# Kernel tuning notes

Measured on AMD Instinct MI355X. Metric: run time of the kernel, lower is better.

Reference implementation:

```python
import jax, jax.numpy as jnp
import numpy as np

D_MODEL = 2048
N_Q = 32
N_KV = 8  # num_heads // 4
HEAD_DIM = D_MODEL // N_Q  # 64
CTX = 2048


def precompute_rope_freqs(head_dim, max_seq_len):
    theta = 1.0 / (10000.0 ** (jnp.arange(0, head_dim, 2, dtype=jnp.float32) / head_dim))
    positions = jnp.arange(max_seq_len, dtype=jnp.float32)
    return jnp.outer(positions, theta)  # [T, head_dim//2]


def apply_rope(x, freqs):
    # x: [B, T, H, D]; freqs: [T, D//2]
    T = x.shape[1]
    f = freqs[:T][None, :, None, :]  # [1, T, 1, D//2]
    cos, sin = jnp.cos(f), jnp.sin(f)
    D = x.shape[-1]
    x1, x2 = x[..., : D // 2], x[..., D // 2 :]
    return jnp.concatenate([x1 * cos - x2 * sin, x1 * sin + x2 * cos], axis=-1)


def setup_inputs() -> dict:
    key = jax.random.key(0)
    ks = jax.random.split(key, 10)
    s = 0.02
    B, T = 1, CTX
    inp = {
        "x": jax.random.normal(ks[0], (B, T, D_MODEL), dtype=jnp.float32),
        "Wq": jax.random.normal(ks[1], (D_MODEL, N_Q * HEAD_DIM), dtype=jnp.float32) * s,
        "bq": jnp.zeros((N_Q * HEAD_DIM,), dtype=jnp.float32),
        "Wk": jax.random.normal(ks[2], (D_MODEL, N_KV * HEAD_DIM), dtype=jnp.float32) * s,
        "bk": jnp.zeros((N_KV * HEAD_DIM,), dtype=jnp.float32),
        "Wv": jax.random.normal(ks[3], (D_MODEL, N_KV * HEAD_DIM), dtype=jnp.float32) * s,
        "bv": jnp.zeros((N_KV * HEAD_DIM,), dtype=jnp.float32),
        "Wo": jax.random.normal(ks[4], (D_MODEL, D_MODEL), dtype=jnp.float32) * s,
        "bo": jnp.zeros((D_MODEL,), dtype=jnp.float32),
        "freqs": precompute_rope_freqs(HEAD_DIM, CTX),
    }
    return inp


def reference(x, Wq, bq, Wk, bk, Wv, bv, Wo, bo, freqs):
    B, T, C = x.shape
    q = (x @ Wq + bq).reshape(B, T, N_Q, HEAD_DIM)
    k = (x @ Wk + bk).reshape(B, T, N_KV, HEAD_DIM)
    v = (x @ Wv + bv).reshape(B, T, N_KV, HEAD_DIM)
    q = apply_rope(q, freqs)
    k = apply_rope(k, freqs)
    repeat = N_Q // N_KV
    # repeat_interleave along head dim: q head h uses kv head h // repeat
    k = jnp.repeat(k, repeat, axis=2)
    v = jnp.repeat(v, repeat, axis=2)
    # [B, H, T, D]
    q = q.transpose(0, 2, 1, 3)
    k = k.transpose(0, 2, 1, 3)
    v = v.transpose(0, 2, 1, 3)
    scale = 1.0 / jnp.sqrt(jnp.asarray(HEAD_DIM, dtype=x.dtype))
    scores = jnp.einsum("bhtd,bhsd->bhts", q, k) * scale  # [B, H, T, T]
    causal = jnp.tril(jnp.ones((T, T), dtype=bool))
    scores = jnp.where(causal[None, None], scores, jnp.finfo(scores.dtype).min)
    attn = jax.nn.softmax(scores, axis=-1)
    out = jnp.einsum("bhts,bhsd->bhtd", attn, v)  # [B, H, T, D]
    out = out.transpose(0, 2, 1, 3).reshape(B, T, C)
    return out @ Wo + bo
```

## Files before the change

### kernel.cpp

```cpp
#include <hip/hip_runtime.h>
#include <hip/hip_bf16.h>
#include <math.h>

#define T_CTX 2048
#define DM    2048
#define NQ    32
#define NKV   8
#define HD    64
#define QKV_LD 3072

typedef __attribute__((ext_vector_type(8))) short short8;
typedef __attribute__((ext_vector_type(4))) float floatx4;

__device__ __forceinline__ void gload_lds16(const void* g, void* l) {
  __builtin_amdgcn_global_load_lds(
      (const __attribute__((address_space(1))) void*)g,
      (__attribute__((address_space(3))) void*)l, 16, 0, 0);
}

__device__ __forceinline__ void tcast_body(const float* __restrict__ src,
                                           __hip_bfloat16* __restrict__ dst,
                                           int Ncols, int Krows, int bx, int by,
                                           int tid, float (*tile)[66]) {
  const int n0 = bx * 64, k0 = by * 64;
  const int c = tid & 63, r0 = tid >> 6;
#pragma unroll
  for (int s = 0; s < 16; ++s) {
    int r = r0 + 4 * s;
    tile[r][c] = src[(size_t)(k0 + r) * Ncols + n0 + c];
  }
  __syncthreads();
#pragma unroll
  for (int s = 0; s < 16; ++s) {
    int r = r0 + 4 * s;
    dst[(size_t)(n0 + r) * Krows + k0 + c] = __float2bfloat16(tile[c][r]);
  }
}

__global__ __launch_bounds__(256) void prep_kernel(
    const float* __restrict__ x, const float* __restrict__ Wq,
    const float* __restrict__ Wk, const float* __restrict__ Wv,
    const float* __restrict__ Wo, const float* __restrict__ bq,
    const float* __restrict__ bk, const float* __restrict__ bv,
    __hip_bfloat16* __restrict__ xb, __hip_bfloat16* __restrict__ wt,
    __hip_bfloat16* __restrict__ wot, float* __restrict__ bcat) {
  __shared__ float tile[64][66];
  const int bid = blockIdx.x;
  const int tid = threadIdx.x;
  if (bid < 2048) {
    const int i = bid * 256 + tid;
    const float4 a = ((const float4*)x)[2 * i];
    const float4 b = ((const float4*)x)[2 * i + 1];
    union { ushort u[8]; short8 v; } o;
    __hip_bfloat16 h;
    h = __float2bfloat16(a.x); o.u[0] = *(ushort*)&h;
    h = __float2bfloat16(a.y); o.u[1] = *(ushort*)&h;
    h = __float2bfloat16(a.z); o.u[2] = *(ushort*)&h;
    h = __float2bfloat16(a.w); o.u[3] = *(ushort*)&h;
    h = __float2bfloat16(b.x); o.u[4] = *(ushort*)&h;
    h = __float2bfloat16(b.y); o.u[5] = *(ushort*)&h;
    h = __float2bfloat16(b.z); o.u[6] = *(ushort*)&h;
    h = __float2bfloat16(b.w); o.u[7] = *(ushort*)&h;
    ((short8*)xb)[i] = o.v;
  } else if (bid < 3072) {
    const int lid = bid - 2048;
    tcast_body(Wq, wt, 2048, 2048, lid & 31, lid >> 5, tid, tile);
  } else if (bid < 3328) {
    const int lid = bid - 3072;
    tcast_body(Wk, wt + (size_t)2048 * 2048, 512, 2048, lid & 7, lid >> 3, tid, tile);
  } else if (bid < 3584) {
    const int lid = bid - 3328;
    tcast_body(Wv, wt + (size_t)2560 * 2048, 512, 2048, lid & 7, lid >> 3, tid, tile);
  } else if (bid < 4608) {
    const int lid = bid - 3584;
    tcast_body(Wo, wot, 2048, 2048, lid & 31, lid >> 5, tid, tile);
  } else {
    for (int i = tid; i < 3072; i += 256)
      bcat[i] = (i < 2048) ? bq[i] : ((i < 2560) ? bk[i - 2048] : bv[i - 2560]);
  }
}

template <typename OutT>
__global__ __launch_bounds__(256) void gemm_mfma_bt(
    const __hip_bfloat16* __restrict__ A, const __hip_bfloat16* __restrict__ Bt,
    const float* __restrict__ bias, OutT* __restrict__ C, int K, int ldc) {
  __shared__ alignas(16) short As[128 * 64];
  __shared__ alignas(16) short Bs[128 * 64];
  const int tid = threadIdx.x;
  const int lane = tid & 63;
  const int w = tid >> 6;
  const int wr = w >> 1, wc = w & 1;
  const int bm = blockIdx.y * 128, bn = blockIdx.x * 128;

  floatx4 acc[4][4];
#pragma unroll
  for (int m = 0; m < 4; ++m)
#pragma unroll
    for (int n = 0; n < 4; ++n) acc[m][n] = floatx4{0.f, 0.f, 0.f, 0.f};

  const int frag_kb = (lane >> 4) * 16;
  const int srow_in8 = lane >> 3;
  const int sbyte = (lane & 7) * 16;

  for (int k0 = 0; k0 < K; k0 += 64) {
    __syncthreads();
#pragma unroll
    for (int i = 0; i < 4; ++i) {
      const int r = w * 32 + i * 8 + srow_in8;
      const int gcb = sbyte ^ ((r & 7) << 4);
      gload_lds16((const char*)(A + (size_t)(bm + r) * K + k0) + gcb,
                  (char*)As + (w * 32 + i * 8) * 128);
      gload_lds16((const char*)(Bt + (size_t)(bn + r) * K + k0) + gcb,
                  (char*)Bs + (w * 32 + i * 8) * 128);
    }
    __syncthreads();
#pragma unroll
    for (int h = 0; h < 2; ++h) {
      short8 af[4], bf[4];
      const int kb = h * 64 + frag_kb;
#pragma unroll
      for (int m = 0; m < 4; ++m) {
        const int ar = wr * 64 + m * 16 + (lane & 15);
        af[m] = *(const short8*)((const char*)As + ar * 128 + (kb ^ ((ar & 7) << 4)));
      }
#pragma unroll
      for (int n = 0; n < 4; ++n) {
        const int br = wc * 64 + n * 16 + (lane & 15);
        bf[n] = *(const short8*)((const char*)Bs + br * 128 + (kb ^ ((br & 7) << 4)));
      }
#pragma unroll
      for (int m = 0; m < 4; ++m)
#pragma unroll
        for (int n = 0; n < 4; ++n)
          acc[m][n] = __builtin_amdgcn_mfma_f32_16x16x32_bf16(af[m], bf[n], acc[m][n], 0, 0, 0);
    }
  }

  const int col_l = lane & 15;
  const int row_l = (lane >> 4) * 4;
#pragma unroll
  for (int n = 0; n < 4; ++n) {
    const int col = bn + wc * 64 + n * 16 + col_l;
    const float bv = bias[col];
#pragma unroll
    for (int m = 0; m < 4; ++m) {
      const int row0 = bm + wr * 64 + m * 16 + row_l;
#pragma unroll
      for (int r2 = 0; r2 < 4; ++r2) {
        const float v = acc[m][n][r2] + bv;
        if constexpr (sizeof(OutT) == 2)
          C[(size_t)(row0 + r2) * ldc + col] = __float2bfloat16(v);
        else
          C[(size_t)(row0 + r2) * ldc + col] = v;
      }
    }
  }
}

__global__ __launch_bounds__(256) void rope_kernel(__hip_bfloat16* __restrict__ qkv,
                                                   const float* __restrict__ freqs) {
  const int idx = blockIdx.x * 256 + threadIdx.x;
  const int i = idx & 31;
  const int h = (idx >> 5) % 40;
  const int t = idx / (40 * 32);
  const int base = (h < 32) ? h * HD : DM + (h - 32) * HD;
  __hip_bfloat16* p = qkv + (size_t)t * QKV_LD + base;
  const float f = freqs[t * 32 + i];
  float s, c;
  sincosf(f, &s, &c);
  const float x1 = __bfloat162float(p[i]);
  const float x2 = __bfloat162float(p[i + 32]);
  float r1 = x1 * c - x2 * s;
  float r2 = x1 * s + x2 * c;
  if (h < 32) { r1 *= 0.125f; r2 *= 0.125f; }
  p[i]      = __float2bfloat16(r1);
  p[i + 32] = __float2bfloat16(r2);
}

__global__ __launch_bounds__(256) void transpose_v_kernel(
    const __hip_bfloat16* __restrict__ qkv, __hip_bfloat16* __restrict__ vt) {
  __shared__ short tile[64][66];
  const int c0 = blockIdx.x * 64;
  const int t0 = blockIdx.y * 64;
  const int c = threadIdx.x & 63;
  const int r0 = threadIdx.x >> 6;
#pragma unroll
  for (int s = 0; s < 16; ++s) {
    int r = r0 + 4 * s;
    tile[r][c] = *(const short*)(qkv + (size_t)(t0 + r) * QKV_LD + DM + NKV * HD + c0 + c);
  }
  __syncthreads();
#pragma unroll
  for (int s = 0; s < 16; ++s) {
    int r = r0 + 4 * s;
    *(short*)(vt + (size_t)(c0 + r) * T_CTX + t0 + c) = tile[c][r];
  }
}

__global__ __launch_bounds__(256) void attn_mfma_kernel(
    const __hip_bfloat16* __restrict__ qkv, const __hip_bfloat16* __restrict__ vtg,
    __hip_bfloat16* __restrict__ O) {
  const int bid = blockIdx.x;
  const int hp = bid >> 5;
  const int qb = 31 - (bid & 31);
  const int h0 = hp * 2;
  const int kvh = h0 >> 2;
  const int tid = threadIdx.x;
  const int lane = tid & 63;
  const int w = tid >> 6;
  const int l15 = lane & 15;
  const int lg = lane >> 4;
  const int qbase = qb * 64 + w * 16;

  __shared__ alignas(16) char Ks[64 * 128];
  __shared__ alignas(16) char Vts[64 * 128];
  __shared__ alignas(16) char Ps[4][2][16 * 128];

  short8 qf[2][2];
#pragma unroll
  for (int hh = 0; hh < 2; ++hh)
#pragma unroll
    for (int kh = 0; kh < 2; ++kh)
      qf[hh][kh] = *(const short8*)(qkv + (size_t)(qbase + l15) * QKV_LD +
                                    (h0 + hh) * HD + kh * 32 + lg * 8);

  floatx4 o_acc[2][4];
  float mrow[2][4], lrow[2][4];
#pragma unroll
  for (int hh = 0; hh < 2; ++hh)
#pragma unroll
    for (int n = 0; n < 4; ++n) o_acc[hh][n] = floatx4{0.f, 0.f, 0.f, 0.f};
#pragma unroll
  for (int hh = 0; hh < 2; ++hh)
#pragma unroll
    for (int r = 0; r < 4; ++r) { mrow[hh][r] = -INFINITY; lrow[hh][r] = 0.f; }

  const __hip_bfloat16* Kg = qkv + DM + kvh * HD;
  const int nt = qb + 1;
  const int srow_in8 = lane >> 3;
  const int sbyte = (lane & 7) * 16;

  for (int kt = 0; kt < nt; ++kt) {
    const int s0 = kt * 64;
    __syncthreads();
#pragma unroll
    for (int i = 0; i < 2; ++i) {
      const int r = w * 16 + i * 8 + srow_in8;
      const int gcb = sbyte ^ ((r & 7) << 4);
      gload_lds16((const char*)(Kg + (size_t)(s0 + r) * QKV_LD) + gcb,
                  Ks + (w * 16 + i * 8) * 128);
      gload_lds16((const char*)(vtg + (size_t)(kvh * 64 + r) * T_CTX + s0) + gcb,
                  Vts + (w * 16 + i * 8) * 128);
    }
    __syncthreads();

    if (s0 > qbase + 15) continue;

    floatx4 sacc[2][4];
#pragma unroll
    for (int hh = 0; hh < 2; ++hh)
#pragma unroll
      for (int n = 0; n < 4; ++n) sacc[hh][n] = floatx4{0.f, 0.f, 0.f, 0.f};
#pragma unroll
    for (int kh = 0; kh < 2; ++kh) {
      short8 bf[4];
#pragma unroll
      for (int n = 0; n < 4; ++n) {
        const int kr = n * 16 + l15;
        bf[n] = *(const short8*)(Ks + kr * 128 + ((kh * 64 + lg * 16) ^ ((kr & 7) << 4)));
      }
#pragma unroll
      for (int hh = 0; hh < 2; ++hh)
#pragma unroll
        for (int n = 0; n < 4; ++n)
          sacc[hh][n] = __builtin_amdgcn_mfma_f32_16x16x32_bf16(qf[hh][kh], bf[n], sacc[hh][n], 0, 0, 0);
    }
    if (s0 + 63 > qbase) {
#pragma unroll
      for (int n = 0; n < 4; ++n)
#pragma unroll
        for (int r = 0; r < 4; ++r)
          if (s0 + n * 16 + l15 > qbase + lg * 4 + r) {
            sacc[0][n][r] = -INFINITY;
            sacc[1][n][r] = -INFINITY;
          }
    }
#pragma unroll
    for (int hh = 0; hh < 2; ++hh) {
#pragma unroll
      for (int r = 0; r < 4; ++r) {
        float t = fmaxf(fmaxf(sacc[hh][0][r], sacc[hh][1][r]),
                        fmaxf(sacc[hh][2][r], sacc[hh][3][r]));
        t = fmaxf(t, __shfl_xor(t, 1));
        t = fmaxf(t, __shfl_xor(t, 2));
        t = fmaxf(t, __shfl_xor(t, 4));
        t = fmaxf(t, __shfl_xor(t, 8));
        float mn = mrow[hh][r];
        if (t > mn + 8.f) {
          const float corr = __expf(mn - t);
          lrow[hh][r] *= corr;
#pragma unroll
          for (int n = 0; n < 4; ++n) o_acc[hh][n][r] *= corr;
          mn = t;
          mrow[hh][r] = t;
        }
        float pv[4];
        float ls = 0.f;
#pragma unroll
        for (int n = 0; n < 4; ++n) {
          pv[n] = __expf(sacc[hh][n][r] - mn);
          ls += pv[n];
        }
        ls += __shfl_xor(ls, 1);
        ls += __shfl_xor(ls, 2);
        ls += __shfl_xor(ls, 4);
        ls += __shfl_xor(ls, 8);
        lrow[hh][r] += ls;
        const int prow = lg * 4 + r;
#pragma unroll
        for (int n = 0; n < 4; ++n)
          *(__hip_bfloat16*)(Ps[w][hh] + prow * 128 +
                             (((n * 16 + l15) * 2) ^ ((prow & 7) << 4))) =
              __float2bfloat16(pv[n]);
      }
    }
#pragma unroll
    for (int kh = 0; kh < 2; ++kh) {
      short8 vf[4];
#pragma unroll
      for (int n = 0; n < 4; ++n) {
        const int vr = n * 16 + l15;
        vf[n] = *(const short8*)(Vts + vr * 128 + ((kh * 64 + lg * 16) ^ ((vr & 7) << 4)));
      }
#pragma unroll
      for (int hh = 0; hh < 2; ++hh) {
        const short8 pf = *(const short8*)(Ps[w][hh] + l15 * 128 +
                                           ((kh * 64 + lg * 16) ^ ((l15 & 7) << 4)));
#pragma unroll
        for (int n = 0; n < 4; ++n)
          o_acc[hh][n] = __builtin_amdgcn_mfma_f32_16x16x32_bf16(pf, vf[n], o_acc[hh][n], 0, 0, 0);
      }
    }
  }

#pragma unroll
  for (int hh = 0; hh < 2; ++hh) {
    float inv[4];
#pragma unroll
    for (int r = 0; r < 4; ++r) inv[r] = 1.f / lrow[hh][r];
#pragma unroll
    for (int n = 0; n < 4; ++n)
#pragma unroll
      for (int r = 0; r < 4; ++r)
        O[(size_t)(qbase + lg * 4 + r) * DM + (h0 + hh) * HD + n * 16 + l15] =
            __float2bfloat16(o_acc[hh][n][r] * inv[r]);
  }
}

extern "C" void kernel_launch(void* const* d_in, const int* in_sizes, int n_in,
                              void* d_out, int out_size, void* d_ws, size_t ws_size,
                              hipStream_t stream) {
  const float* x     = (const float*)d_in[0];
  const float* Wq    = (const float*)d_in[1];
  const float* bq    = (const float*)d_in[2];
  const float* Wk    = (const float*)d_in[3];
  const float* bk    = (const float*)d_in[4];
  const float* Wv    = (const float*)d_in[5];
  const float* bv    = (const float*)d_in[6];
  const float* Wo    = (const float*)d_in[7];
  const float* bo    = (const float*)d_in[8];
  const float* freqs = (const float*)d_in[9];
  float* out = (float*)d_out;

  char* ws = (char*)d_ws;
  __hip_bfloat16* qkv  = (__hip_bfloat16*)ws;
  __hip_bfloat16* wt   = (__hip_bfloat16*)(ws + 12582912);
  __hip_bfloat16* xb   = (__hip_bfloat16*)(ws + 25165824);
  __hip_bfloat16* obuf = xb;
  __hip_bfloat16* wot  = (__hip_bfloat16*)(ws + 33554432);
  __hip_bfloat16* vt   = (__hip_bfloat16*)(ws + 41943040);
  float*          bcat = (float*)(ws + 44040192);

  const dim3 blk(256);

  prep_kernel<<<dim3(4609), blk, 0, stream>>>(x, Wq, Wk, Wv, Wo, bq, bk, bv,
                                              xb, wt, wot, bcat);

  gemm_mfma_bt<__hip_bfloat16><<<dim3(3072 / 128, 2048 / 128), blk, 0, stream>>>(
      xb, wt, bcat, qkv, DM, QKV_LD);

  rope_kernel<<<(T_CTX * 40 * 32) / 256, blk, 0, stream>>>(qkv, freqs);

  transpose_v_kernel<<<dim3(8, 32), blk, 0, stream>>>(qkv, vt);

  attn_mfma_kernel<<<dim3(16 * 32), blk, 0, stream>>>(qkv, vt, obuf);

  gemm_mfma_bt<float><<<dim3(2048 / 128, 2048 / 128), blk, 0, stream>>>(
      obuf, wot, bo, out, DM, DM);
}
```

Baseline: 314.8 us.

## Double-buffer GEMM LDS tiles and split long causal attention rows across blocks

The GEMM now double-buffers its A/B LDS tiles, issuing the next tile's global-to-LDS loads before computing on the current one, with a single barrier per iteration. The attention kernel splits the upper 16 query blocks' KV range into two halves handled by separate blocks (768 blocks instead of 512). Each half writes unnormalized partial outputs plus row max and sum, and a new combine kernel merges them. This targets load imbalance from causal masking and memory latency in the GEMM, at the cost of an extra launch, partial-result traffic and doubled GEMM LDS use (64KB), which may reduce occupancy.

```diff
diff --git a/kernel.cpp b/kernel.cpp
--- a/kernel.cpp
+++ b/kernel.cpp
@@ -84,8 +84,8 @@
 __global__ __launch_bounds__(256) void gemm_mfma_bt(
     const __hip_bfloat16* __restrict__ A, const __hip_bfloat16* __restrict__ Bt,
     const float* __restrict__ bias, OutT* __restrict__ C, int K, int ldc) {
-  __shared__ alignas(16) short As[128 * 64];
-  __shared__ alignas(16) short Bs[128 * 64];
+  __shared__ alignas(16) short As[2][128 * 64];
+  __shared__ alignas(16) short Bs[2][128 * 64];
   const int tid = threadIdx.x;
   const int lane = tid & 63;
   const int w = tid >> 6;
@@ -99,21 +99,26 @@
     for (int n = 0; n < 4; ++n) acc[m][n] = floatx4{0.f, 0.f, 0.f, 0.f};
 
   const int frag_kb = (lane >> 4) * 16;
-  const int srow_in8 = lane >> 3;
+  const int srow8 = lane >> 3;
   const int sbyte = (lane & 7) * 16;
 
-  for (int k0 = 0; k0 < K; k0 += 64) {
-    __syncthreads();
+  auto stage = [&](int buf, int k0) {
 #pragma unroll
     for (int i = 0; i < 4; ++i) {
-      const int r = w * 32 + i * 8 + srow_in8;
+      const int r = w * 32 + i * 8 + srow8;
       const int gcb = sbyte ^ ((r & 7) << 4);
       gload_lds16((const char*)(A + (size_t)(bm + r) * K + k0) + gcb,
-                  (char*)As + (w * 32 + i * 8) * 128);
+                  (char*)(As[buf]) + (w * 32 + i * 8) * 128);
       gload_lds16((const char*)(Bt + (size_t)(bn + r) * K + k0) + gcb,
-                  (char*)Bs + (w * 32 + i * 8) * 128);
-    }
-    __syncthreads();
+                  (char*)(Bs[buf]) + (w * 32 + i * 8) * 128);
+    }
+  };
+
+  stage(0, 0);
+  __syncthreads();
+  int cur = 0;
+  for (int k0 = 0; k0 < K; k0 += 64) {
+    if (k0 + 64 < K) stage(cur ^ 1, k0 + 64);
 #pragma unroll
     for (int h = 0; h < 2; ++h) {
       short8 af[4], bf[4];
@@ -121,12 +126,12 @@
 #pragma unroll
       for (int m = 0; m < 4; ++m) {
         const int ar = wr * 64 + m * 16 + (lane & 15);
-        af[m] = *(const short8*)((const char*)As + ar * 128 + (kb ^ ((ar & 7) << 4)));
+        af[m] = *(const short8*)((const char*)(As[cur]) + ar * 128 + (kb ^ ((ar & 7) << 4)));
       }
 #pragma unroll
       for (int n = 0; n < 4; ++n) {
         const int br = wc * 64 + n * 16 + (lane & 15);
-        bf[n] = *(const short8*)((const char*)Bs + br * 128 + (kb ^ ((br & 7) << 4)));
+        bf[n] = *(const short8*)((const char*)(Bs[cur]) + br * 128 + (kb ^ ((br & 7) << 4)));
       }
 #pragma unroll
       for (int m = 0; m < 4; ++m)
@@ -134,6 +139,8 @@
         for (int n = 0; n < 4; ++n)
           acc[m][n] = __builtin_amdgcn_mfma_f32_16x16x32_bf16(af[m], bf[n], acc[m][n], 0, 0, 0);
     }
+    __syncthreads();
+    cur ^= 1;
   }
 
   const int col_l = lane & 15;
@@ -199,10 +206,25 @@
 
 __global__ __launch_bounds__(256) void attn_mfma_kernel(
     const __hip_bfloat16* __restrict__ qkv, const __hip_bfloat16* __restrict__ vtg,
-    __hip_bfloat16* __restrict__ O) {
+    __hip_bfloat16* __restrict__ O, __hip_bfloat16* __restrict__ Opart,
+    float* __restrict__ mlpart) {
   const int bid = blockIdx.x;
-  const int hp = bid >> 5;
-  const int qb = 31 - (bid & 31);
+  const int hp = bid / 48;
+  const int w48 = bid % 48;
+  int qb, t0, t1, half;
+  bool split;
+  if (w48 < 32) {
+    qb = 31 - (w48 >> 1);
+    half = w48 & 1;
+    const int h = (qb + 2) >> 1;
+    split = true;
+    t0 = half ? h : 0;
+    t1 = half ? (qb + 1) : h;
+  } else {
+    qb = 15 - (w48 - 32);
+    half = 0; split = false;
+    t0 = 0; t1 = qb + 1;
+  }
   const int h0 = hp * 2;
   const int kvh = h0 >> 2;
   const int tid = threadIdx.x;
@@ -236,16 +258,15 @@
     for (int r = 0; r < 4; ++r) { mrow[hh][r] = -INFINITY; lrow[hh][r] = 0.f; }
 
   const __hip_bfloat16* Kg = qkv + DM + kvh * HD;
-  const int nt = qb + 1;
-  const int srow_in8 = lane >> 3;
+  const int srow8 = lane >> 3;
   const int sbyte = (lane & 7) * 16;
 
-  for (int kt = 0; kt < nt; ++kt) {
+  for (int kt = t0; kt < t1; ++kt) {
     const int s0 = kt * 64;
     __syncthreads();
 #pragma unroll
     for (int i = 0; i < 2; ++i) {
-      const int r = w * 16 + i * 8 + srow_in8;
+      const int r = w * 16 + i * 8 + srow8;
       const int gcb = sbyte ^ ((r & 7) << 4);
       gload_lds16((const char*)(Kg + (size_t)(s0 + r) * QKV_LD) + gcb,
                   Ks + (w * 16 + i * 8) * 128);
@@ -343,18 +364,63 @@
     }
   }
 
-#pragma unroll
-  for (int hh = 0; hh < 2; ++hh) {
-    float inv[4];
-#pragma unroll
-    for (int r = 0; r < 4; ++r) inv[r] = 1.f / lrow[hh][r];
-#pragma unroll
-    for (int n = 0; n < 4; ++n)
-#pragma unroll
-      for (int r = 0; r < 4; ++r)
-        O[(size_t)(qbase + lg * 4 + r) * DM + (h0 + hh) * HD + n * 16 + l15] =
-            __float2bfloat16(o_acc[hh][n][r] * inv[r]);
-  }
+  if (!split) {
+#pragma unroll
+    for (int hh = 0; hh < 2; ++hh) {
+      float inv[4];
+#pragma unroll
+      for (int r = 0; r < 4; ++r) inv[r] = 1.f / lrow[hh][r];
+#pragma unroll
+      for (int n = 0; n < 4; ++n)
+#pragma unroll
+        for (int r = 0; r < 4; ++r)
+          O[(size_t)(qbase + lg * 4 + r) * DM + (h0 + hh) * HD + n * 16 + l15] =
+              __float2bfloat16(o_acc[hh][n][r] * inv[r]);
+    }
+  } else {
+#pragma unroll
+    for (int hh = 0; hh < 2; ++hh) {
+      const int u = (((h0 + hh) << 4) + (qb - 16)) * 2 + half;
+#pragma unroll
+      for (int n = 0; n < 4; ++n)
+#pragma unroll
+        for (int r = 0; r < 4; ++r)
+          Opart[(size_t)u * 4096 + (w * 16 + lg * 4 + r) * 64 + n * 16 + l15] =
+              __float2bfloat16(o_acc[hh][n][r]);
+      if (l15 == 0) {
+#pragma unroll
+        for (int r = 0; r < 4; ++r) {
+          mlpart[u * 128 + w * 16 + lg * 4 + r]      = mrow[hh][r];
+          mlpart[u * 128 + 64 + w * 16 + lg * 4 + r] = lrow[hh][r];
+        }
+      }
+    }
+  }
+}
+
+__global__ __launch_bounds__(256) void combine_kernel(
+    const __hip_bfloat16* __restrict__ Opart, const float* __restrict__ mlpart,
+    __hip_bfloat16* __restrict__ O) {
+  const int head = blockIdx.x >> 4;
+  const int sqb = blockIdx.x & 15;
+  const int tid = threadIdx.x;
+  const int r = tid >> 2;
+  const int c0 = (tid & 3) * 16;
+  const int u0 = (((head << 4) + sqb) << 1);
+  const float m0 = mlpart[u0 * 128 + r];
+  const float l0 = mlpart[u0 * 128 + 64 + r];
+  const float m1 = mlpart[(u0 + 1) * 128 + r];
+  const float l1 = mlpart[(u0 + 1) * 128 + 64 + r];
+  const float M = fmaxf(m0, m1);
+  const float a0 = __expf(m0 - M), a1 = __expf(m1 - M);
+  const float inv = 1.f / (a0 * l0 + a1 * l1);
+  const __hip_bfloat16* p0 = Opart + (size_t)u0 * 4096 + r * 64 + c0;
+  const __hip_bfloat16* p1 = Opart + (size_t)(u0 + 1) * 4096 + r * 64 + c0;
+  __hip_bfloat16* op = O + (size_t)((16 + sqb) * 64 + r) * DM + head * HD + c0;
+#pragma unroll
+  for (int j = 0; j < 16; ++j)
+    op[j] = __float2bfloat16(
+        (a0 * __bfloat162float(p0[j]) + a1 * __bfloat162float(p1[j])) * inv);
 }
 
 extern "C" void kernel_launch(void* const* d_in, const int* in_sizes, int n_in,
@@ -373,13 +439,15 @@
   float* out = (float*)d_out;
 
   char* ws = (char*)d_ws;
-  __hip_bfloat16* qkv  = (__hip_bfloat16*)ws;
-  __hip_bfloat16* wt   = (__hip_bfloat16*)(ws + 12582912);
-  __hip_bfloat16* xb   = (__hip_bfloat16*)(ws + 25165824);
-  __hip_bfloat16* obuf = xb;
-  __hip_bfloat16* wot  = (__hip_bfloat16*)(ws + 33554432);
-  __hip_bfloat16* vt   = (__hip_bfloat16*)(ws + 41943040);
-  float*          bcat = (float*)(ws + 44040192);
+  __hip_bfloat16* qkv   = (__hip_bfloat16*)ws;
+  __hip_bfloat16* wt    = (__hip_bfloat16*)(ws + 12582912);
+  __hip_bfloat16* obuf  = wt;
+  __hip_bfloat16* xb    = (__hip_bfloat16*)(ws + 25165824);
+  __hip_bfloat16* opart = xb;
+  __hip_bfloat16* wot   = (__hip_bfloat16*)(ws + 33554432);
+  __hip_bfloat16* vt    = (__hip_bfloat16*)(ws + 41943040);
+  float*          bcat  = (float*)(ws + 44040192);
+  float*          ml    = (float*)(ws + 44052480);
 
   const dim3 blk(256);
 
@@ -393,7 +461,8 @@
 
   transpose_v_kernel<<<dim3(8, 32), blk, 0, stream>>>(qkv, vt);
 
-  attn_mfma_kernel<<<dim3(16 * 32), blk, 0, stream>>>(qkv, vt, obuf);
+  attn_mfma_kernel<<<dim3(16 * 48), blk, 0, stream>>>(qkv, vt, obuf, opart, ml);
+  combine_kernel<<<dim3(512), blk, 0, stream>>>(opart, ml, obuf);
 
   gemm_mfma_bt<float><<<dim3(2048 / 128, 2048 / 128), blk, 0, stream>>>(
       obuf, wot, bo, out, DM, DM);
```

Result: faster. 302.0 us (-4.0%).
